# Kernel optimization log

Measured on AMD Instinct MI355X. Metric: run time of the kernel, lower is better.

Reference implementation:

```python
import jax, jax.numpy as jnp
import numpy as np

N, IN_DIM, OUT_DIM, HEADS = 8192, 256, 128, 2


def setup_inputs() -> dict:
    key = jax.random.key(0)
    k1, k2, k3, k4, k5 = jax.random.split(key, 5)
    features = jax.random.normal(k1, (N, IN_DIM), dtype=jnp.float32)
    adjacency = jax.random.randint(k2, (N, N), 0, 2, dtype=jnp.int32)
    # nn.Linear(input_dim, output_dim*heads, bias=False): weight [out, in]
    W = jax.random.normal(k3, (OUT_DIM * HEADS, IN_DIM), dtype=jnp.float32) * 0.05
    attn_src = jax.random.normal(k4, (HEADS, OUT_DIM), dtype=jnp.float32) * 0.05
    attn_dst = jax.random.normal(k5, (HEADS, OUT_DIM), dtype=jnp.float32) * 0.05
    return {"features": features, "adjacency": adjacency, "W": W,
            "attn_src": attn_src, "attn_dst": attn_dst}


def reference(features, adjacency, W, attn_src, attn_dst):
    n = features.shape[0]
    # transformed: [N, H, F]
    transformed = (features @ W.T).reshape(n, HEADS, OUT_DIM)
    src_scores = jnp.einsum('nhf,hf->nh', transformed, attn_src)  # [N, H]
    dst_scores = jnp.einsum('nhf,hf->nh', transformed, attn_dst)  # [N, H]
    # logits: [N_src, N_dst, H]
    logits = jax.nn.leaky_relu(src_scores[:, None, :] + dst_scores[None, :, :],
                               negative_slope=0.2)
    mask = adjacency > 0  # [N, N]
    logits = jnp.where(mask[:, :, None], logits, -jnp.inf)
    attention = jax.nn.softmax(logits, axis=1)  # softmax over dst dim (dim=1)
    attention = jnp.nan_to_num(attention, nan=0.0, posinf=0.0, neginf=0.0)
    aggregated = jnp.einsum('ijh,jhf->ihf', attention, transformed)  # [N, H, F]
    return aggregated.mean(axis=1)  # [N, F]
```

## Files before the change

kernel.cpp:

```cpp
#include <hip/hip_runtime.h>
#include <stdint.h>
#include <stddef.h>

#define NN 8192
#define KD 256
#define CD 256
#define FD 128
#define BI 64
#define BJ 64

typedef __attribute__((ext_vector_type(4))) float f32x4;
typedef __attribute__((ext_vector_type(8))) short b16x8;

__device__ __forceinline__ unsigned short f2bf(float x) {
    unsigned int u = __float_as_uint(x);
    u += 0x7fffu + ((u >> 16) & 1u);
    return (unsigned short)(u >> 16);
}

__device__ __forceinline__ unsigned int cvtpk(float lo, float hi) {
    unsigned int r;
    asm("v_cvt_pk_bf16_f32 %0, %1, %2" : "=v"(r) : "v"(lo), "v"(hi));
    return r;
}

__device__ __forceinline__ void async16(const void* g, void* l) {
    __builtin_amdgcn_global_load_lds(
        (const __attribute__((address_space(1))) unsigned int*)g,
        (__attribute__((address_space(3))) unsigned int*)l, 16, 0, 0);
}

__global__ __launch_bounds__(256) void k_transform(
    const float* __restrict__ feat, const float* __restrict__ W,
    const float* __restrict__ asrc, const float* __restrict__ adst,
    unsigned short* __restrict__ Tt, float* __restrict__ s, float* __restrict__ d)
{
    __shared__ unsigned short a_lds[64 * 32];
    __shared__ unsigned short b_lds[256 * 32];
    __shared__ unsigned short tr_lds[256 * 72];
    __shared__ float sc_lds[4][64];
    __shared__ float dc_lds[4][64];

    const int t = threadIdx.x;
    const int wave = t >> 6, lane = t & 63;
    const int l15 = lane & 15, quad = lane >> 4;
    const int n0 = blockIdx.x * 64;
    const int ai = t >> 2, ag = t & 3;

    f32x4 acc[4][4] = {};
    for (int kc = 0; kc < 8; ++kc) {
        const int k0 = kc * 32;
        __syncthreads();
        {
            const float* src = feat + (size_t)(n0 + ai) * KD + k0 + ag * 8;
            const float4 v0 = *(const float4*)src;
            const float4 v1 = *(const float4*)(src + 4);
            union { unsigned int u[4]; b16x8 v; } pk;
            pk.u[0] = cvtpk(v0.x, v0.y); pk.u[1] = cvtpk(v0.z, v0.w);
            pk.u[2] = cvtpk(v1.x, v1.y); pk.u[3] = cvtpk(v1.z, v1.w);
            const int slot = ag ^ ((ai >> 1) & 3);
            *(b16x8*)&a_lds[ai * 32 + slot * 8] = pk.v;
        }
        for (int p = 0; p < 4; ++p) {
            const int G = p * 256 + t;
            const int c = G >> 2, g = G & 3;
            const float* src = W + (size_t)c * KD + k0 + g * 8;
            const float4 v0 = *(const float4*)src;
            const float4 v1 = *(const float4*)(src + 4);
            union { unsigned int u[4]; b16x8 v; } pk;
            pk.u[0] = cvtpk(v0.x, v0.y); pk.u[1] = cvtpk(v0.z, v0.w);
            pk.u[2] = cvtpk(v1.x, v1.y); pk.u[3] = cvtpk(v1.z, v1.w);
            const int slot = g ^ ((c >> 1) & 3);
            *(b16x8*)&b_lds[c * 32 + slot * 8] = pk.v;
        }
        __syncthreads();
        b16x8 af[4], bfr[4];
        for (int mt = 0; mt < 4; ++mt) {
            const int m = mt * 16 + l15;
            af[mt] = *(const b16x8*)&a_lds[m * 32 + (quad ^ ((m >> 1) & 3)) * 8];
        }
        for (int nt = 0; nt < 4; ++nt) {
            const int c = wave * 64 + nt * 16 + l15;
            bfr[nt] = *(const b16x8*)&b_lds[c * 32 + (quad ^ ((c >> 1) & 3)) * 8];
        }
        for (int mt = 0; mt < 4; ++mt)
            for (int nt = 0; nt < 4; ++nt)
                acc[mt][nt] = __builtin_amdgcn_mfma_f32_16x16x32_bf16(
                    af[mt], bfr[nt], acc[mt][nt], 0, 0, 0);
    }

    float aS[4], aD[4];
    for (int nt = 0; nt < 4; ++nt) {
        const int c = wave * 64 + nt * 16 + l15;
        aS[nt] = asrc[c]; aD[nt] = adst[c];
    }
    for (int mt = 0; mt < 4; ++mt)
        for (int r = 0; r < 4; ++r) {
            float vs = 0.f, vd = 0.f;
            for (int nt = 0; nt < 4; ++nt) {
                const float x = acc[mt][nt][r];
                vs += x * aS[nt]; vd += x * aD[nt];
            }
            vs += __shfl_xor(vs, 1); vd += __shfl_xor(vd, 1);
            vs += __shfl_xor(vs, 2); vd += __shfl_xor(vd, 2);
            vs += __shfl_xor(vs, 4); vd += __shfl_xor(vd, 4);
            vs += __shfl_xor(vs, 8); vd += __shfl_xor(vd, 8);
            if (l15 == 0) {
                const int nl = mt * 16 + quad * 4 + r;
                sc_lds[wave][nl] = vs; dc_lds[wave][nl] = vd;
            }
        }
    for (int mt = 0; mt < 4; ++mt)
        for (int nt = 0; nt < 4; ++nt) {
            const int c = wave * 64 + nt * 16 + l15;
            const int n = mt * 16 + quad * 4;
            *(unsigned int*)&tr_lds[c * 72 + n] =
                cvtpk(acc[mt][nt][0], acc[mt][nt][1]);
            *(unsigned int*)&tr_lds[c * 72 + n + 2] =
                cvtpk(acc[mt][nt][2], acc[mt][nt][3]);
        }
    __syncthreads();
    if (t < 128) {
        const int n = t >> 1, h = t & 1;
        s[(size_t)(n0 + n) * 2 + h] = sc_lds[h * 2][n] + sc_lds[h * 2 + 1][n];
        d[(size_t)(n0 + n) * 2 + h] = dc_lds[h * 2][n] + dc_lds[h * 2 + 1][n];
    }
    for (int p = 0; p < 8; ++p) {
        const int idx = p * 256 + t;
        const int c = idx >> 3, g = idx & 7;
        *(b16x8*)(Tt + (size_t)c * NN + n0 + g * 8) = *(const b16x8*)&tr_lds[c * 72 + g * 8];
    }
}

__global__ __launch_bounds__(512, 4) void k_gat(
    const int* __restrict__ adj, const unsigned short* __restrict__ Tt,
    const float* __restrict__ s, const float* __restrict__ d,
    float* __restrict__ num_part,
    float* __restrict__ den_part,
    int jchunk)
{
    __shared__ unsigned short tt_lds[2][CD * BJ];
    __shared__ unsigned short w_lds[2 * BI * BJ];

    const int t = threadIdx.x;
    const int w = t >> 6, lane = t & 63;
    const int l15 = lane & 15, quad = lane >> 4;
    const int h  = (w >> 2) & 1;
    const int fh = (w >> 1) & 1;
    const int rh = w & 1;
    const int i0 = blockIdx.x * BI;
    const int chunk = blockIdx.y;
    const int jbase = chunk * jchunk;

    const int wi = t >> 3;
    const int j8 = t & 7;
    const int gi = i0 + wi;
    const float s0 = s[(size_t)gi * 2 + 0];
    const float s1 = s[(size_t)gi * 2 + 1];
    const int cbase = h * 128 + fh * 64;

    f32x4 acc[2][4] = {};
    float den0 = 0.f, den1 = 0.f;
    const int njt = jchunk / BJ;

    const int* arow = adj + (size_t)gi * NN + j8 * 8;
    const float* drow = d + (size_t)j8 * 16;
    const int c0 = w * 8 + (lane >> 3);
    const int g0 = (lane & 7) ^ (c0 & 7);
    const unsigned short* tsrc0 = Tt + (size_t)c0 * NN + g0 * 8;
    const int toff0 = w * 1024;
    const int slot = (j8 ^ (wi & 7)) << 3;
    unsigned short* wp0 = &w_lds[(0 * BI + wi) * BJ + slot];
    const int m0 = rh * 32 + l15;
    const int afb = (h * BI + m0) * BJ;
    const int bfb = (cbase + l15) * BJ;
    const int X0 = ((0 * 4 + quad) ^ (l15 & 7)) << 3;
    const int X1 = ((1 * 4 + quad) ^ (l15 & 7)) << 3;
    const int X[2] = {X0, X1};

    #pragma unroll
    for (int p = 0; p < 4; ++p)
        async16(tsrc0 + (size_t)p * 64 * NN + jbase,
                (char*)&tt_lds[0][0] + toff0 + p * 8192);
    int4 aA0 = *(const int4*)(arow + jbase);
    int4 aA1 = *(const int4*)(arow + jbase + 4);
    const float4* dpp = (const float4*)(drow + 2 * jbase);
    float4 dA0 = dpp[0], dA1 = dpp[1], dA2 = dpp[2], dA3 = dpp[3];
    int4 aB0, aB1; float4 dB0, dB1, dB2, dB3;

    auto body = [&](int jt, int buf,
                    int4& ca0, int4& ca1, float4& cd0, float4& cd1, float4& cd2, float4& cd3,
                    int4& na0, int4& na1, float4& nd0, float4& nd1, float4& nd2, float4& nd3) {
        const int j0 = jbase + jt * BJ;
        __builtin_amdgcn_s_barrier();
        const int jn = (jt + 1 < njt) ? j0 + BJ : j0;
        #pragma unroll
        for (int p = 0; p < 4; ++p)
            async16(tsrc0 + (size_t)p * 64 * NN + jn,
                    (char*)&tt_lds[buf ^ 1][0] + toff0 + p * 8192);
        na0 = *(const int4*)(arow + jn);
        na1 = *(const int4*)(arow + jn + 4);
        { const float4* dnp = (const float4*)(drow + 2 * jn);
          nd0 = dnp[0]; nd1 = dnp[1]; nd2 = dnp[2]; nd3 = dnp[3]; }
        union { float4 v[4]; float f[16]; } dv;
        dv.v[0] = cd0; dv.v[1] = cd1; dv.v[2] = cd2; dv.v[3] = cd3;
        const int am[8] = {ca0.x, ca0.y, ca0.z, ca0.w, ca1.x, ca1.y, ca1.z, ca1.w};
        float e0f[8], e1f[8];
        float dp0 = 0.f, dp1 = 0.f;
        #pragma unroll
        for (int e = 0; e < 8; ++e) {
            float x0 = s0 + dv.f[e * 2 + 0];  x0 = fmaxf(x0, 0.2f * x0);
            float x1 = s1 + dv.f[e * 2 + 1];  x1 = fmaxf(x1, 0.2f * x1);
            e0f[e] = am[e] != 0 ? __expf(x0) : 0.f;
            e1f[e] = am[e] != 0 ? __expf(x1) : 0.f;
            dp0 += e0f[e]; dp1 += e1f[e];
        }
        den0 += dp0; den1 += dp1;
        union { unsigned int u[4]; b16x8 v; } w0, w1;
        #pragma unroll
        for (int q = 0; q < 4; ++q) {
            w0.u[q] = cvtpk(e0f[2 * q], e0f[2 * q + 1]);
            w1.u[q] = cvtpk(e1f[2 * q], e1f[2 * q + 1]);
        }
        *(b16x8*)wp0 = w0.v;
        *(b16x8*)(wp0 + BI * BJ) = w1.v;
        asm volatile("s_waitcnt vmcnt(10) lgkmcnt(0)" ::: "memory");
        __builtin_amdgcn_s_barrier();
        __builtin_amdgcn_sched_barrier(0);
        #pragma unroll
        for (int ks = 0; ks < 2; ++ks) {
            b16x8 af[2], bf[4];
            #pragma unroll
            for (int mt = 0; mt < 2; ++mt)
                af[mt] = *(const b16x8*)&w_lds[afb + mt * 1024 + X[ks]];
            #pragma unroll
            for (int nt = 0; nt < 4; ++nt)
                bf[nt] = *(const b16x8*)&tt_lds[buf][bfb + nt * 1024 + X[ks]];
            #pragma unroll
            for (int mt = 0; mt < 2; ++mt)
                #pragma unroll
                for (int nt = 0; nt < 4; ++nt)
                    acc[mt][nt] = __builtin_amdgcn_mfma_f32_16x16x32_bf16(
                        af[mt], bf[nt], acc[mt][nt], 0, 0, 0);
        }
    };

    for (int jt = 0; jt < njt; jt += 2) {
        body(jt,     0, aA0, aA1, dA0, dA1, dA2, dA3, aB0, aB1, dB0, dB1, dB2, dB3);
        body(jt + 1, 1, aB0, aB1, dB0, dB1, dB2, dB3, aA0, aA1, dA0, dA1, dA2, dA3);
    }
    asm volatile("s_waitcnt vmcnt(0)" ::: "memory");
    den0 += __shfl_xor(den0, 1); den0 += __shfl_xor(den0, 2); den0 += __shfl_xor(den0, 4);
    den1 += __shfl_xor(den1, 1); den1 += __shfl_xor(den1, 2); den1 += __shfl_xor(den1, 4);
    if (j8 == 0) {
        den_part[((size_t)chunk * 2 + 0) * NN + gi] = den0;
        den_part[((size_t)chunk * 2 + 1) * NN + gi] = den1;
    }
    float* np_ = num_part + (size_t)chunk * NN * CD;
    for (int mt = 0; mt < 2; ++mt)
        for (int nt = 0; nt < 4; ++nt)
            for (int r = 0; r < 4; ++r) {
                const int n = i0 + rh * 32 + mt * 16 + quad * 4 + r;
                const int c = cbase + nt * 16 + l15;
                np_[(size_t)n * CD + c] = acc[mt][nt][r];
            }
}

__global__ __launch_bounds__(256) void k_combine(
    const float* __restrict__ num_part, const float* __restrict__ den_part,
    float* __restrict__ out, int jsplit)
{
    const int idx = blockIdx.x * 256 + threadIdx.x;
    const int n = idx >> 7, f = idx & 127;
    const size_t row = (size_t)n * CD;
    float n0 = 0.f, n1 = 0.f, d0 = 0.f, d1 = 0.f;
    for (int c = 0; c < jsplit; ++c) {
        const size_t base = (size_t)c * NN * CD;
        n0 += num_part[base + row + f];
        n1 += num_part[base + row + 128 + f];
        d0 += den_part[((size_t)c * 2 + 0) * NN + n];
        d1 += den_part[((size_t)c * 2 + 1) * NN + n];
    }
    const float r0 = d0 != 0.f ? n0 / d0 : 0.f;
    const float r1 = d1 != 0.f ? n1 / d1 : 0.f;
    out[idx] = 0.5f * (r0 + r1);
}

extern "C" void kernel_launch(void* const* d_in, const int* in_sizes, int n_in,
                              void* d_out, int out_size, void* d_ws, size_t ws_size,
                              hipStream_t stream) {
    const float* feat = (const float*)d_in[0];
    const int*   adj  = (const int*)d_in[1];
    const float* W    = (const float*)d_in[2];
    const float* asrc = (const float*)d_in[3];
    const float* adst = (const float*)d_in[4];
    float* out = (float*)d_out;

    const int jsplit = (ws_size >= ((size_t)40 << 20)) ? 4 : 2;
    const int jchunk = NN / jsplit;

    char* ws = (char*)d_ws;
    unsigned short* Tt = (unsigned short*)ws;
    float* s    = (float*)(ws + ((size_t)4 << 20));
    float* dsc  = (float*)(ws + ((size_t)4 << 20) + (64 << 10));
    float* den  = (float*)(ws + ((size_t)4 << 20) + (128 << 10));
    float* nump = (float*)(ws + ((size_t)8 << 20));

    k_transform<<<128, 256, 0, stream>>>(feat, W, asrc, adst, Tt, s, dsc);
    k_gat<<<dim3(NN / BI, jsplit), 512, 0, stream>>>(adj, Tt, s, dsc, nump, den, jchunk);
    k_combine<<<NN * FD / 256, 256, 0, stream>>>(nump, den, out, jsplit);
}
```

Before: 438.3 us.

## Halve transform tile, prescale scores by log2e, use raw exp2 and setprio

The transform kernel now processes 32 rows per block instead of 64, which doubles the grid to 256 blocks for better CU coverage. Source and destination scores are prescaled by log2(e) so the attention kernel can call the raw v_exp_f32 instruction instead of __expf. The leaky-relu and exp math is rewritten on float2 vectors. s_setprio is raised around the MFMA section so waves reaching the matrix work get scheduling priority. Numerics shift slightly because the prescale is applied before leaky-relu, which is fine since leaky-relu scales linearly.

```diff
diff --git a/kernel.cpp b/kernel.cpp
--- a/kernel.cpp
+++ b/kernel.cpp
@@ -8,19 +8,21 @@
 #define FD 128
 #define BI 64
 #define BJ 64
+#define LOG2E 1.44269504f
 
 typedef __attribute__((ext_vector_type(4))) float f32x4;
+typedef __attribute__((ext_vector_type(2))) float f32x2;
 typedef __attribute__((ext_vector_type(8))) short b16x8;
-
-__device__ __forceinline__ unsigned short f2bf(float x) {
-    unsigned int u = __float_as_uint(x);
-    u += 0x7fffu + ((u >> 16) & 1u);
-    return (unsigned short)(u >> 16);
-}
 
 __device__ __forceinline__ unsigned int cvtpk(float lo, float hi) {
     unsigned int r;
     asm("v_cvt_pk_bf16_f32 %0, %1, %2" : "=v"(r) : "v"(lo), "v"(hi));
+    return r;
+}
+
+__device__ __forceinline__ float exp2raw(float x) {
+    float r;
+    asm("v_exp_f32 %0, %1\n\ts_nop 0" : "=v"(r) : "v"(x));
     return r;
 }
 
@@ -35,23 +37,23 @@
     const float* __restrict__ asrc, const float* __restrict__ adst,
     unsigned short* __restrict__ Tt, float* __restrict__ s, float* __restrict__ d)
 {
-    __shared__ unsigned short a_lds[64 * 32];
+    __shared__ unsigned short a_lds[32 * 32];
     __shared__ unsigned short b_lds[256 * 32];
-    __shared__ unsigned short tr_lds[256 * 72];
-    __shared__ float sc_lds[4][64];
-    __shared__ float dc_lds[4][64];
+    __shared__ unsigned short tr_lds[256 * 40];
+    __shared__ float sc_lds[4][32];
+    __shared__ float dc_lds[4][32];
 
     const int t = threadIdx.x;
     const int wave = t >> 6, lane = t & 63;
     const int l15 = lane & 15, quad = lane >> 4;
-    const int n0 = blockIdx.x * 64;
-    const int ai = t >> 2, ag = t & 3;
-
-    f32x4 acc[4][4] = {};
+    const int n0 = blockIdx.x * 32;
+
+    f32x4 acc[2][4] = {};
     for (int kc = 0; kc < 8; ++kc) {
         const int k0 = kc * 32;
         __syncthreads();
-        {
+        if (t < 128) {
+            const int ai = t >> 2, ag = t & 3;
             const float* src = feat + (size_t)(n0 + ai) * KD + k0 + ag * 8;
             const float4 v0 = *(const float4*)src;
             const float4 v1 = *(const float4*)(src + 4);
@@ -74,8 +76,8 @@
             *(b16x8*)&b_lds[c * 32 + slot * 8] = pk.v;
         }
         __syncthreads();
-        b16x8 af[4], bfr[4];
-        for (int mt = 0; mt < 4; ++mt) {
+        b16x8 af[2], bfr[4];
+        for (int mt = 0; mt < 2; ++mt) {
             const int m = mt * 16 + l15;
             af[mt] = *(const b16x8*)&a_lds[m * 32 + (quad ^ ((m >> 1) & 3)) * 8];
         }
@@ -83,7 +85,7 @@
             const int c = wave * 64 + nt * 16 + l15;
             bfr[nt] = *(const b16x8*)&b_lds[c * 32 + (quad ^ ((c >> 1) & 3)) * 8];
         }
-        for (int mt = 0; mt < 4; ++mt)
+        for (int mt = 0; mt < 2; ++mt)
             for (int nt = 0; nt < 4; ++nt)
                 acc[mt][nt] = __builtin_amdgcn_mfma_f32_16x16x32_bf16(
                     af[mt], bfr[nt], acc[mt][nt], 0, 0, 0);
@@ -94,7 +96,7 @@
         const int c = wave * 64 + nt * 16 + l15;
         aS[nt] = asrc[c]; aD[nt] = adst[c];
     }
-    for (int mt = 0; mt < 4; ++mt)
+    for (int mt = 0; mt < 2; ++mt)
         for (int r = 0; r < 4; ++r) {
             float vs = 0.f, vd = 0.f;
             for (int nt = 0; nt < 4; ++nt) {
@@ -110,25 +112,25 @@
                 sc_lds[wave][nl] = vs; dc_lds[wave][nl] = vd;
             }
         }
-    for (int mt = 0; mt < 4; ++mt)
+    for (int mt = 0; mt < 2; ++mt)
         for (int nt = 0; nt < 4; ++nt) {
             const int c = wave * 64 + nt * 16 + l15;
             const int n = mt * 16 + quad * 4;
-            *(unsigned int*)&tr_lds[c * 72 + n] =
+            *(unsigned int*)&tr_lds[c * 40 + n] =
                 cvtpk(acc[mt][nt][0], acc[mt][nt][1]);
-            *(unsigned int*)&tr_lds[c * 72 + n + 2] =
+            *(unsigned int*)&tr_lds[c * 40 + n + 2] =
                 cvtpk(acc[mt][nt][2], acc[mt][nt][3]);
         }
     __syncthreads();
-    if (t < 128) {
+    if (t < 64) {
         const int n = t >> 1, h = t & 1;
-        s[(size_t)(n0 + n) * 2 + h] = sc_lds[h * 2][n] + sc_lds[h * 2 + 1][n];
-        d[(size_t)(n0 + n) * 2 + h] = dc_lds[h * 2][n] + dc_lds[h * 2 + 1][n];
-    }
-    for (int p = 0; p < 8; ++p) {
+        s[(size_t)(n0 + n) * 2 + h] = (sc_lds[h * 2][n] + sc_lds[h * 2 + 1][n]) * LOG2E;
+        d[(size_t)(n0 + n) * 2 + h] = (dc_lds[h * 2][n] + dc_lds[h * 2 + 1][n]) * LOG2E;
+    }
+    for (int p = 0; p < 4; ++p) {
         const int idx = p * 256 + t;
-        const int c = idx >> 3, g = idx & 7;
-        *(b16x8*)(Tt + (size_t)c * NN + n0 + g * 8) = *(const b16x8*)&tr_lds[c * 72 + g * 8];
+        const int c = idx >> 2, g = idx & 3;
+        *(b16x8*)(Tt + (size_t)c * NN + n0 + g * 8) = *(const b16x8*)&tr_lds[c * 40 + g * 8];
     }
 }
 
@@ -155,8 +157,7 @@
     const int wi = t >> 3;
     const int j8 = t & 7;
     const int gi = i0 + wi;
-    const float s0 = s[(size_t)gi * 2 + 0];
-    const float s1 = s[(size_t)gi * 2 + 1];
+    const f32x2 s01 = *(const f32x2*)(s + (size_t)gi * 2);
     const int cbase = h * 128 + fh * 64;
 
     f32x4 acc[2][4] = {};
@@ -174,9 +175,8 @@
     const int m0 = rh * 32 + l15;
     const int afb = (h * BI + m0) * BJ;
     const int bfb = (cbase + l15) * BJ;
-    const int X0 = ((0 * 4 + quad) ^ (l15 & 7)) << 3;
-    const int X1 = ((1 * 4 + quad) ^ (l15 & 7)) << 3;
-    const int X[2] = {X0, X1};
+    const int X[2] = {((0 * 4 + quad) ^ (l15 & 7)) << 3,
+                      ((1 * 4 + quad) ^ (l15 & 7)) << 3};
 
     #pragma unroll
     for (int p = 0; p < 4; ++p)
@@ -202,31 +202,32 @@
         na1 = *(const int4*)(arow + jn + 4);
         { const float4* dnp = (const float4*)(drow + 2 * jn);
           nd0 = dnp[0]; nd1 = dnp[1]; nd2 = dnp[2]; nd3 = dnp[3]; }
-        union { float4 v[4]; float f[16]; } dv;
+        union { float4 v[4]; f32x2 p[8]; } dv;
         dv.v[0] = cd0; dv.v[1] = cd1; dv.v[2] = cd2; dv.v[3] = cd3;
         const int am[8] = {ca0.x, ca0.y, ca0.z, ca0.w, ca1.x, ca1.y, ca1.z, ca1.w};
-        float e0f[8], e1f[8];
-        float dp0 = 0.f, dp1 = 0.f;
+        f32x2 ef[8];
+        f32x2 dp = {0.f, 0.f};
         #pragma unroll
         for (int e = 0; e < 8; ++e) {
-            float x0 = s0 + dv.f[e * 2 + 0];  x0 = fmaxf(x0, 0.2f * x0);
-            float x1 = s1 + dv.f[e * 2 + 1];  x1 = fmaxf(x1, 0.2f * x1);
-            e0f[e] = am[e] != 0 ? __expf(x0) : 0.f;
-            e1f[e] = am[e] != 0 ? __expf(x1) : 0.f;
-            dp0 += e0f[e]; dp1 += e1f[e];
-        }
-        den0 += dp0; den1 += dp1;
+            const f32x2 x = s01 + dv.p[e];
+            const f32x2 xm = __builtin_elementwise_max(x, 0.2f * x);
+            const float r0 = exp2raw(xm.x), r1 = exp2raw(xm.y);
+            const f32x2 em = {am[e] != 0 ? r0 : 0.f, am[e] != 0 ? r1 : 0.f};
+            ef[e] = em; dp += em;
+        }
+        den0 += dp.x; den1 += dp.y;
         union { unsigned int u[4]; b16x8 v; } w0, w1;
         #pragma unroll
         for (int q = 0; q < 4; ++q) {
-            w0.u[q] = cvtpk(e0f[2 * q], e0f[2 * q + 1]);
-            w1.u[q] = cvtpk(e1f[2 * q], e1f[2 * q + 1]);
+            w0.u[q] = cvtpk(ef[2 * q].x, ef[2 * q + 1].x);
+            w1.u[q] = cvtpk(ef[2 * q].y, ef[2 * q + 1].y);
         }
         *(b16x8*)wp0 = w0.v;
         *(b16x8*)(wp0 + BI * BJ) = w1.v;
         asm volatile("s_waitcnt vmcnt(10) lgkmcnt(0)" ::: "memory");
         __builtin_amdgcn_s_barrier();
         __builtin_amdgcn_sched_barrier(0);
+        __builtin_amdgcn_s_setprio(1);
         #pragma unroll
         for (int ks = 0; ks < 2; ++ks) {
             b16x8 af[2], bf[4];
@@ -243,6 +244,7 @@
                     acc[mt][nt] = __builtin_amdgcn_mfma_f32_16x16x32_bf16(
                         af[mt], bf[nt], acc[mt][nt], 0, 0, 0);
         }
+        __builtin_amdgcn_s_setprio(0);
     };
 
     for (int jt = 0; jt < njt; jt += 2) {
@@ -306,7 +308,7 @@
     float* den  = (float*)(ws + ((size_t)4 << 20) + (128 << 10));
     float* nump = (float*)(ws + ((size_t)8 << 20));
 
-    k_transform<<<128, 256, 0, stream>>>(feat, W, asrc, adst, Tt, s, dsc);
+    k_transform<<<256, 256, 0, stream>>>(feat, W, asrc, adst, Tt, s, dsc);
     k_gat<<<dim3(NN / BI, jsplit), 512, 0, stream>>>(adj, Tt, s, dsc, nump, den, jchunk);
     k_combine<<<NN * FD / 256, 256, 0, stream>>>(nump, den, out, jsplit);
 }
```

Result: no change. 435.6 us (median of 2 runs) (-0.6%).
